# Performance work log

Measured on AMD Instinct MI355X. Metric: run time of the kernel, lower is better.

Reference implementation:

```python
import jax, jax.numpy as jnp
import numpy as np

B, T, C, K, V = 4, 4096, 128, 64, 64
EPS = 1e-5


def layer_norm(x, g, b):
    mu = jnp.mean(x, axis=-1, keepdims=True)
    var = jnp.var(x, axis=-1, keepdims=True)
    return (x - mu) * jax.lax.rsqrt(var + EPS) * g + b


def setup_inputs() -> dict:
    key = jax.random.key(0)
    ks = jax.random.split(key, 8)
    s = 1.0 / np.sqrt(C)
    return {
        "x": jax.random.normal(ks[0], (B, T, C), dtype=jnp.float32),
        "Wq": jax.random.uniform(ks[1], (C, K), jnp.float32, -s, s),
        "bq": jnp.zeros((K,), jnp.float32),
        "Wk": jax.random.uniform(ks[2], (C, K), jnp.float32, -s, s),
        "bk": jnp.zeros((K,), jnp.float32),
        "Wv": jax.random.uniform(ks[3], (C, V), jnp.float32, -s, s),
        "bv": jnp.zeros((V,), jnp.float32),
        "gq": jnp.ones((K,), jnp.float32), "bgq": jnp.zeros((K,), jnp.float32),
        "gk": jnp.ones((K,), jnp.float32), "bgk": jnp.zeros((K,), jnp.float32),
        "gv": jnp.ones((V,), jnp.float32), "bgv": jnp.zeros((V,), jnp.float32),
        "go": jnp.ones((V,), jnp.float32), "bgo": jnp.zeros((V,), jnp.float32),
    }


def reference(x, Wq, bq, Wk, bk, Wv, bv, gq, bgq, gk, bgk, gv, bgv, go, bgo):
    # projections: B x T x {K,K,V}
    q = layer_norm(x @ Wq + bq, gq, bgq)
    k = layer_norm(x @ Wk + bk, gk, bgk)
    v = layer_norm(x @ Wv + bv, gv, bgv)
    sqrt_k = jnp.asarray(np.sqrt(K), x.dtype)
    # full B x T x T causal score matrix (faithful to the original bmm+mask)
    logits = jnp.einsum("btk,bsk->bts", q, k) / sqrt_k
    t = jnp.arange(T)
    causal = t[:, None] >= t[None, :]  # lower-triangular incl. diagonal
    logits = jnp.where(causal[None], logits, -jnp.inf)
    probs = jax.nn.softmax(logits, axis=-1)
    read = jnp.einsum("bts,bsv->btv", probs, v)
    read = layer_norm(read, go, bgo)
    return jnp.concatenate([x, read], axis=2)  # B x T x (C+V)
```

## Files before the change

kernel.cpp:

```cpp
#include <hip/hip_runtime.h>

#define TT 4096

typedef unsigned short u16;
typedef unsigned int u32;

typedef short bf16x8 __attribute__((ext_vector_type(8)));
typedef float f32x4 __attribute__((ext_vector_type(4)));

union U8 {
  uint2 q[2];
  uint4 u4;
  bf16x8 v;
  short s[8];
  u32 w[4];
};

static __device__ __forceinline__ u16 f2bf(float f) {
  union { float f; u32 u; } cv;
  cv.f = f;
  u32 r = cv.u + 0x7FFFu + ((cv.u >> 16) & 1u);
  return (u16)(r >> 16);
}
static __device__ __forceinline__ u32 pk2(float a, float b) {
  return (u32)f2bf(a) | ((u32)f2bf(b) << 16);
}
static __device__ __forceinline__ float bf2f(u16 h) {
  union { u32 u; float f; } cv;
  cv.u = ((u32)h) << 16;
  return cv.f;
}
static __device__ __forceinline__ float exp2a(float x) {
  float r; asm("v_exp_f32 %0, %1" : "=v"(r) : "v"(x)); return r;
}
static __device__ __forceinline__ u32 cvtpk(float lo, float hi) {
  u32 r; asm("v_cvt_pk_bf16_f32 %0, %1, %2" : "=v"(r) : "v"(lo), "v"(hi)); return r;
}

__global__ __launch_bounds__(64)
void wpack(const float* __restrict__ Wq, const float* __restrict__ Wk,
           const float* __restrict__ Wv, u16* __restrict__ wf)
{
  const int g = blockIdx.x;
  const int p = g >> 4, s = (g >> 2) & 3, nt = g & 3;
  const int l = threadIdx.x, lg = l >> 4, l15 = l & 15;
  const float* W = (p == 0) ? Wq : (p == 1) ? Wk : Wv;
  const int n = l15 + 16 * nt;
  U8 o;
#pragma unroll
  for (int j = 0; j < 8; ++j) {
    int k = 32 * s + ((j < 4) ? (4 * lg + j) : (16 + 4 * lg + (j - 4)));
    o.s[j] = (short)f2bf(W[k * 64 + n]);
  }
  *(uint4*)(wf + (size_t)(g * 64 + l) * 8) = o.u4;
}

__global__ __launch_bounds__(256)
void proj_mfma(const float* __restrict__ x, const u16* __restrict__ wf,
               const float* __restrict__ bq, const float* __restrict__ bk,
               const float* __restrict__ bv,
               const float* __restrict__ gq, const float* __restrict__ bgq,
               const float* __restrict__ gk, const float* __restrict__ bgk,
               const float* __restrict__ gv, const float* __restrict__ bgv,
               u16* __restrict__ qo, u16* __restrict__ ko, u16* __restrict__ vto,
               float* __restrict__ out)
{
  __shared__ u16 xs[64 * 130];
  const int bx = blockIdx.x;
  const int xcd = bx & 7, i = bx >> 3;
  const int tile = xcd * 32 + (i & 31);
  const int p = i >> 5;
  const int rowbase = tile * 64;
  const int t = threadIdx.x;

  {
    const int row = t >> 2, seg = t & 3;
    const float4* src = (const float4*)(x + (size_t)(rowbase + row) * 128 + seg * 32);
    float4 f[8];
#pragma unroll
    for (int q = 0; q < 8; ++q) f[q] = src[q];
    if ((p == 0 && seg < 2) || (p == 1 && seg >= 2)) {
      float4* dst = (float4*)(out + (size_t)(rowbase + row) * 192 + seg * 32);
#pragma unroll
      for (int q = 0; q < 8; ++q) dst[q] = f[q];
    }
    const int base = row * 256 + seg * 64;
    const int swz = (row & 7) << 4;
    char* xb = (char*)xs;
#pragma unroll
    for (int q = 0; q < 4; ++q) {
      uint4 u;
      u.x = pk2(f[2 * q].x, f[2 * q].y);
      u.y = pk2(f[2 * q].z, f[2 * q].w);
      u.z = pk2(f[2 * q + 1].x, f[2 * q + 1].y);
      u.w = pk2(f[2 * q + 1].z, f[2 * q + 1].w);
      *(uint4*)(xb + ((base + 16 * q) ^ swz)) = u;
    }
  }

  const int w = t >> 6, l = t & 63, lg = l >> 4, l15 = l & 15;
  U8 bfr[4][4];
  const u16* wp = wf + (size_t)p * (16 * 64 * 8);
#pragma unroll
  for (int s = 0; s < 4; ++s)
#pragma unroll
    for (int nt = 0; nt < 4; ++nt)
      bfr[s][nt].u4 = *(const uint4*)(wp + ((s * 4 + nt) * 64 + l) * 8);

  __syncthreads();

  f32x4 acc[4];
#pragma unroll
  for (int nt = 0; nt < 4; ++nt) acc[nt] = (f32x4){0.f, 0.f, 0.f, 0.f};
  const int abase = (16 * w + l15) * 256;
  const int aswz = (l15 & 7) << 4;
  const char* xb = (const char*)xs;
#pragma unroll
  for (int s = 0; s < 4; ++s) {
    U8 af;
    af.q[0] = *(const uint2*)(xb + ((abase + s * 64 + 8 * lg) ^ aswz));
    af.q[1] = *(const uint2*)(xb + ((abase + s * 64 + 8 * lg + 32) ^ aswz));
#pragma unroll
    for (int nt = 0; nt < 4; ++nt)
      acc[nt] = __builtin_amdgcn_mfma_f32_16x16x32_bf16(af.v, bfr[s][nt].v, acc[nt], 0, 0, 0);
  }

  const float* bb = (p == 0) ? bq : (p == 1) ? bk : bv;
  const float* gg = (p == 0) ? gq : (p == 1) ? gk : gv;
  const float* hh = (p == 0) ? bgq : (p == 1) ? bgk : bgv;
  float bcol[4], gcol[4], hcol[4];
#pragma unroll
  for (int nt = 0; nt < 4; ++nt) {
    int col = l15 + 16 * nt;
    bcol[nt] = bb[col]; gcol[nt] = gg[col]; hcol[nt] = hh[col];
  }
  float vals[4][4];
#pragma unroll
  for (int nt = 0; nt < 4; ++nt)
#pragma unroll
    for (int r = 0; r < 4; ++r) vals[nt][r] = acc[nt][r] + bcol[nt];

  float s1[4], s2[4];
#pragma unroll
  for (int r = 0; r < 4; ++r) {
    s1[r] = vals[0][r] + vals[1][r] + vals[2][r] + vals[3][r];
    s2[r] = vals[0][r] * vals[0][r] + vals[1][r] * vals[1][r]
          + vals[2][r] * vals[2][r] + vals[3][r] * vals[3][r];
#pragma unroll
    for (int d = 1; d < 16; d <<= 1) {
      s1[r] += __shfl_xor(s1[r], d);
      s2[r] += __shfl_xor(s2[r], d);
    }
  }

  if (p < 2) {
    u16* dst = (p == 0) ? qo : ko;
#pragma unroll
    for (int r = 0; r < 4; ++r) {
      float mu = s1[r] * (1.f / 64.f);
      float var = s2[r] * (1.f / 64.f) - mu * mu;
      float rs = rsqrtf(var + 1e-5f);
      int grow = rowbase + 16 * w + 4 * lg + r;
#pragma unroll
      for (int nt = 0; nt < 4; ++nt)
        dst[(size_t)grow * 64 + l15 + 16 * nt] =
            f2bf((vals[nt][r] - mu) * rs * gcol[nt] + hcol[nt]);
    }
  } else {
    u16* vls = xs;
    __syncthreads();
#pragma unroll
    for (int r = 0; r < 4; ++r) {
      float mu = s1[r] * (1.f / 64.f);
      float var = s2[r] * (1.f / 64.f) - mu * mu;
      float rs = rsqrtf(var + 1e-5f);
      int row = 16 * w + 4 * lg + r;
#pragma unroll
      for (int nt = 0; nt < 4; ++nt)
        vls[row * 65 + l15 + 16 * nt] =
            f2bf((vals[nt][r] - mu) * rs * gcol[nt] + hcol[nt]);
    }
    __syncthreads();
    const int b = rowbase >> 12;
    const int tl = rowbase & 4095;
    const int col = t >> 2;
    const int tq = (t & 3) * 16;
    U8 o0, o1;
#pragma unroll
    for (int i = 0; i < 8; ++i) o0.s[i] = (short)vls[(tq + i) * 65 + col];
#pragma unroll
    for (int i = 0; i < 8; ++i) o1.s[i] = (short)vls[(tq + 8 + i) * 65 + col];
    u16* dst = vto + (size_t)(b * 64 + col) * TT + tl + tq;
    *(uint4*)(dst + 0) = o0.u4;
    *(uint4*)(dst + 8) = o1.u4;
  }
}

__global__ __launch_bounds__(256)
void attn_seg4p(const u16* __restrict__ qg, const u16* __restrict__ kg,
                const u16* __restrict__ vtg,
                float* __restrict__ lP, u16* __restrict__ aP)
{
  __shared__ u16 kl4[4 * 64 * 64];
  __shared__ u16 vl4[4 * 64 * 64];
  const int bx = blockIdx.x;
  const int xcd = bx & 7, b = xcd >> 1, e2 = xcd & 1;
  const int j = e2 * 272 + (bx >> 3);
  int Q = 0;
  while (2 * (Q + 1) * (Q + 2) <= j) ++Q;
  const int ip = j - 2 * Q * (Q + 1);
  const int dv = ip / (Q + 1);
  const int q = 4 * Q + dv;
  const int s = ip - dv * (Q + 1);
  const int q0 = q * 64;
  const int it0 = s * 4;
  const int it1 = min(it0 + 4, q + 1);

  const int t = threadIdx.x;
  const int w = t >> 6, l = t & 63;
  const int l15 = l & 15, lg = l >> 4;
  const int swzl = (l15 & 7) << 4;

  const int wbase = q0 + 16 * w;
  const int qrow = wbase + l15;
  const u16* qrp = qg + (size_t)(b * TT + qrow) * 64;
  U8 qf[2];
#pragma unroll
  for (int hh = 0; hh < 2; ++hh) {
    qf[hh].q[0] = *(const uint2*)(qrp + 32 * hh + 4 * lg);
    qf[hh].q[1] = *(const uint2*)(qrp + 32 * hh + 4 * lg + 16);
  }

  {
    const int key = t >> 2, part = t & 3;
    const int sbase = key * 128 + part * 32;
    const int ssw = (key & 7) << 4;
    uint4 kr[4][2], vr[4][2];
#pragma unroll
    for (int tt = 0; tt < 4; ++tt) {
      int tile = it0 + tt; if (tile >= it1) tile = it1 - 1;
      const u16* ks = kg + (size_t)(b * TT + tile * 64 + key) * 64 + part * 16;
      kr[tt][0] = ((const uint4*)ks)[0];
      kr[tt][1] = ((const uint4*)ks)[1];
      const u16* vs = vtg + (size_t)(b * 64 + key) * TT + tile * 64 + part * 16;
      vr[tt][0] = ((const uint4*)vs)[0];
      vr[tt][1] = ((const uint4*)vs)[1];
    }
#pragma unroll
    for (int tt = 0; tt < 4; ++tt) {
      char* kd = (char*)kl4 + tt * 8192;
      char* vd = (char*)vl4 + tt * 8192;
      *(uint4*)(kd + ((sbase + 0) ^ ssw)) = kr[tt][0];
      *(uint4*)(kd + ((sbase + 16) ^ ssw)) = kr[tt][1];
      *(uint4*)(vd + ((sbase + 0) ^ ssw)) = vr[tt][0];
      *(uint4*)(vd + ((sbase + 16) ^ ssw)) = vr[tt][1];
    }
  }
  __syncthreads();

  const float C = 0.18033688011112042f;
  float l_run = 0.f;
  f32x4 acc[4];
#pragma unroll
  for (int ct = 0; ct < 4; ++ct) acc[ct] = (f32x4){0.f, 0.f, 0.f, 0.f};

#define QK_TILE(ST, TOF)                                                      \
  {                                                                           \
    const char* kp_ = (const char*)kl4 + (TOF);                               \
    _Pragma("unroll")                                                         \
    for (int t4 = 0; t4 < 4; ++t4) {                                          \
      const int rbase = (16 * t4 + l15) * 128 + 8 * lg;                       \
      U8 kf0, kf1;                                                            \
      kf0.q[0] = *(const uint2*)(kp_ + ((rbase + 0) ^ swzl));                 \
      kf0.q[1] = *(const uint2*)(kp_ + ((rbase + 32) ^ swzl));                \
      kf1.q[0] = *(const uint2*)(kp_ + ((rbase + 64) ^ swzl));                \
      kf1.q[1] = *(const uint2*)(kp_ + ((rbase + 96) ^ swzl));                \
      f32x4 d_ = {0.f, 0.f, 0.f, 0.f};                                       \
      d_ = __builtin_amdgcn_mfma_f32_16x16x32_bf16(kf0.v, qf[0].v, d_, 0, 0, 0); \
      d_ = __builtin_amdgcn_mfma_f32_16x16x32_bf16(kf1.v, qf[1].v, d_, 0, 0, 0); \
      ST[t4] = d_;                                                            \
    }                                                                         \
  }

  f32x4 stC[4];
  QK_TILE(stC, 0);

  int toff = 0;
  for (int it = it0; it < it1; ++it, toff += 8192) {
    const int kb = it * 64;
    const bool have_next = (it + 1 < it1);

    f32x4 stN[4];
    if (have_next) QK_TILE(stN, toff + 8192);

    const char* vp = (const char*)vl4 + toff;
    U8 vf[4][2];
#pragma unroll
    for (int ct = 0; ct < 4; ++ct) {
      const int vb = (16 * ct + l15) * 128 + 8 * lg;
#pragma unroll
      for (int u = 0; u < 2; ++u) {
        vf[ct][u].q[0] = *(const uint2*)(vp + ((vb + 64 * u + 0) ^ swzl));
        vf[ct][u].q[1] = *(const uint2*)(vp + ((vb + 64 * u + 32) ^ swzl));
      }
    }

    float p[16];
    const bool needmask = (kb + 63 > wbase);
    if (needmask) {
#pragma unroll
      for (int t4 = 0; t4 < 4; ++t4) {
#pragma unroll
        for (int r = 0; r < 4; ++r) {
          int keyidx = kb + 16 * t4 + 4 * lg + r;
          float e = exp2a(stC[t4][r] * C);
          p[t4 * 4 + r] = (keyidx > qrow) ? 0.f : e;
        }
      }
    } else {
#pragma unroll
      for (int t4 = 0; t4 < 4; ++t4) {
#pragma unroll
        for (int r = 0; r < 4; ++r) p[t4 * 4 + r] = exp2a(stC[t4][r] * C);
      }
    }
    float sm[8];
#pragma unroll
    for (int i = 0; i < 8; ++i) sm[i] = p[2 * i] + p[2 * i + 1];
#pragma unroll
    for (int i = 0; i < 4; ++i) sm[i] = sm[2 * i] + sm[2 * i + 1];
    float rsum = (sm[0] + sm[1]) + (sm[2] + sm[3]);
    rsum += __shfl_xor(rsum, 16);
    rsum += __shfl_xor(rsum, 32);
    l_run += rsum;

    U8 pa[2];
#pragma unroll
    for (int u = 0; u < 2; ++u) {
#pragma unroll
      for (int k2 = 0; k2 < 4; ++k2)
        pa[u].w[k2] = cvtpk(p[8 * u + 2 * k2], p[8 * u + 2 * k2 + 1]);
    }

    __builtin_amdgcn_s_setprio(1);
#pragma unroll
    for (int ct = 0; ct < 4; ++ct) {
#pragma unroll
      for (int u = 0; u < 2; ++u)
        acc[ct] = __builtin_amdgcn_mfma_f32_16x16x32_bf16(pa[u].v, vf[ct][u].v, acc[ct], 0, 0, 0);
    }
    __builtin_amdgcn_s_setprio(0);

    if (have_next) {
#pragma unroll
      for (int t4 = 0; t4 < 4; ++t4) stC[t4] = stN[t4];
    }
  }
#undef QK_TILE

  const size_t pbase = (size_t)(b * 544 + j) * 64;
  if (lg == 0) lP[pbase + 16 * w + l15] = l_run;
#pragma unroll
  for (int ct = 0; ct < 4; ++ct) {
#pragma unroll
    for (int r = 0; r < 4; ++r) {
      int rin = 16 * w + 4 * lg + r;
      aP[(pbase + rin) * 64 + l15 + 16 * ct] = f2bf(acc[ct][r]);
    }
  }
}

__global__ __launch_bounds__(256)
void attn_merge4n(const float* __restrict__ lP, const u16* __restrict__ aP,
                  const float* __restrict__ go, const float* __restrict__ bgo,
                  float* __restrict__ out)
{
  const int t = threadIdx.x;
  const int w = t >> 6, c = t & 63;
  const int row = blockIdx.x * 4 + w;
  const int tid2 = row >> 6, rin = row & 63;
  const int b = tid2 >> 6, q = tid2 & 63;
  const int Q = q >> 2;
  const int base_q = b * 544 + 2 * Q * (Q + 1) + (q & 3) * (Q + 1);
  const int ns = Q + 1;

  float L = 0.f, o = 0.f;
  for (int s = 0; s < ns; ++s) {
    const size_t pb = (size_t)(base_q + s) * 64;
    L += lP[pb + rin];
    o += bf2f(aP[(pb + rin) * 64 + c]);
  }
  o /= L;

  float s1 = o, s2 = o * o;
#pragma unroll
  for (int d = 1; d < 64; d <<= 1) {
    s1 += __shfl_xor(s1, d);
    s2 += __shfl_xor(s2, d);
  }
  float mu = s1 * (1.f / 64.f);
  float var = s2 * (1.f / 64.f) - mu * mu;
  float rs = rsqrtf(var + 1e-5f);
  out[(size_t)row * 192 + 128 + c] = (o - mu) * rs * go[c] + bgo[c];
}

__global__ __launch_bounds__(128)
void attn1(const u16* __restrict__ qg, const u16* __restrict__ kg,
           const u16* __restrict__ vtg,
           const float* __restrict__ go, const float* __restrict__ bgo,
           float* __restrict__ out)
{
  __shared__ u16 kl[64 * 64];
  __shared__ u16 vl[64 * 64];
  const int bx = blockIdx.x;
  const int tt = (bx < 256) ? bx : (767 - bx);
  const int b = tt >> 7;
  const int q0 = (tt & 127) * 32;
  const int tid = threadIdx.x;
  const int w = tid >> 6;
  const int l = tid & 63;
  const int l15 = l & 15;
  const int lg = l >> 4;
  const int swzl = (l15 & 7) << 4;

  const int qrow = q0 + 16 * w + l15;
  const u16* qrp = qg + (size_t)(b * TT + qrow) * 64;
  U8 qf[2];
#pragma unroll
  for (int h = 0; h < 2; ++h) {
    qf[h].q[0] = *(const uint2*)(qrp + 32 * h + 4 * lg);
    qf[h].q[1] = *(const uint2*)(qrp + 32 * h + 4 * lg + 16);
  }

  float m_run = -1e30f, l_run = 0.f;
  f32x4 acc[4];
#pragma unroll
  for (int ct = 0; ct < 4; ++ct) acc[ct] = (f32x4){0.f, 0.f, 0.f, 0.f};

  const int nkv = (q0 >> 6) + 1;
  for (int it = 0; it < nkv; ++it) {
    const int kb = it * 64;
    {
      const int key = tid >> 1;
      const int dh = (tid & 1) * 32;
      const u16* ks = kg + (size_t)(b * TT + kb + key) * 64 + dh;
      uint4 d0 = *(const uint4*)(ks + 0);
      uint4 d1 = *(const uint4*)(ks + 8);
      uint4 d2 = *(const uint4*)(ks + 16);
      uint4 d3 = *(const uint4*)(ks + 24);
      const int base = key * 128 + dh * 2;
      const int sw = (key & 7) << 4;
      char* kd = (char*)kl;
      *(uint4*)(kd + ((base + 0) ^ sw)) = d0;
      *(uint4*)(kd + ((base + 16) ^ sw)) = d1;
      *(uint4*)(kd + ((base + 32) ^ sw)) = d2;
      *(uint4*)(kd + ((base + 48) ^ sw)) = d3;
      const u16* vs = vtg + (size_t)(b * 64 + key) * TT + kb + dh;
      uint4 e0 = *(const uint4*)(vs + 0);
      uint4 e1 = *(const uint4*)(vs + 8);
      uint4 e2 = *(const uint4*)(vs + 16);
      uint4 e3 = *(const uint4*)(vs + 24);
      char* vd = (char*)vl;
      *(uint4*)(vd + ((base + 0) ^ sw)) = e0;
      *(uint4*)(vd + ((base + 16) ^ sw)) = e1;
      *(uint4*)(vd + ((base + 32) ^ sw)) = e2;
      *(uint4*)(vd + ((base + 48) ^ sw)) = e3;
    }
    __syncthreads();

    f32x4 st[4];
#pragma unroll
    for (int t4 = 0; t4 < 4; ++t4) {
      const int rbase = (16 * t4 + l15) * 128 + 8 * lg;
      const char* kp = (const char*)kl;
      U8 kf0, kf1;
      kf0.q[0] = *(const uint2*)(kp + ((rbase + 0) ^ swzl));
      kf0.q[1] = *(const uint2*)(kp + ((rbase + 32) ^ swzl));
      kf1.q[0] = *(const uint2*)(kp + ((rbase + 64) ^ swzl));
      kf1.q[1] = *(const uint2*)(kp + ((rbase + 96) ^ swzl));
      f32x4 d = {0.f, 0.f, 0.f, 0.f};
      d = __builtin_amdgcn_mfma_f32_16x16x32_bf16(kf0.v, qf[0].v, d, 0, 0, 0);
      d = __builtin_amdgcn_mfma_f32_16x16x32_bf16(kf1.v, qf[1].v, d, 0, 0, 0);
      st[t4] = d;
    }

    float sv[16];
    const bool needmask = (kb + 63 > q0 + 16 * w);
#pragma unroll
    for (int t4 = 0; t4 < 4; ++t4) {
#pragma unroll
      for (int r = 0; r < 4; ++r) {
        float sc = st[t4][r] * 0.125f;
        if (needmask) {
          int keyidx = kb + 16 * t4 + 4 * lg + r;
          if (keyidx > qrow) sc = -1e30f;
        }
        sv[t4 * 4 + r] = sc;
      }
    }
    float mt = sv[0];
#pragma unroll
    for (int i = 1; i < 16; ++i) mt = fmaxf(mt, sv[i]);
    mt = fmaxf(mt, __shfl_xor(mt, 16));
    mt = fmaxf(mt, __shfl_xor(mt, 32));
    const float mnew = fmaxf(m_run, mt);
    const float al = __expf(m_run - mnew);
    float p[16];
    float rsum = 0.f;
#pragma unroll
    for (int i = 0; i < 16; ++i) { p[i] = __expf(sv[i] - mnew); rsum += p[i]; }
    rsum += __shfl_xor(rsum, 16);
    rsum += __shfl_xor(rsum, 32);
    l_run = l_run * al + rsum;
    m_run = mnew;
    float ar[4];
#pragma unroll
    for (int r = 0; r < 4; ++r) ar[r] = __shfl(al, 4 * lg + r);
#pragma unroll
    for (int ct = 0; ct < 4; ++ct) {
#pragma unroll
      for (int r = 0; r < 4; ++r) acc[ct][r] *= ar[r];
    }
    U8 pa[2];
#pragma unroll
    for (int u = 0; u < 2; ++u) {
#pragma unroll
      for (int i = 0; i < 8; ++i) pa[u].s[i] = (short)f2bf(p[8 * u + i]);
    }

#pragma unroll
    for (int ct = 0; ct < 4; ++ct) {
      const int vb = (16 * ct + l15) * 128 + 8 * lg;
      const char* vp = (const char*)vl;
#pragma unroll
      for (int u = 0; u < 2; ++u) {
        U8 vf;
        vf.q[0] = *(const uint2*)(vp + ((vb + 64 * u + 0) ^ swzl));
        vf.q[1] = *(const uint2*)(vp + ((vb + 64 * u + 32) ^ swzl));
        acc[ct] = __builtin_amdgcn_mfma_f32_16x16x32_bf16(pa[u].v, vf.v, acc[ct], 0, 0, 0);
      }
    }
    __syncthreads();
  }

  float linv[4];
#pragma unroll
  for (int r = 0; r < 4; ++r) linv[r] = 1.f / __shfl(l_run, 4 * lg + r);
  float o[4][4];
#pragma unroll
  for (int ct = 0; ct < 4; ++ct) {
#pragma unroll
    for (int r = 0; r < 4; ++r) o[ct][r] = acc[ct][r] * linv[r];
  }
  float s1[4], s2[4];
#pragma unroll
  for (int r = 0; r < 4; ++r) {
    s1[r] = o[0][r] + o[1][r] + o[2][r] + o[3][r];
    s2[r] = o[0][r] * o[0][r] + o[1][r] * o[1][r] + o[2][r] * o[2][r] + o[3][r] * o[3][r];
#pragma unroll
    for (int d = 1; d < 16; d <<= 1) {
      s1[r] += __shfl_xor(s1[r], d);
      s2[r] += __shfl_xor(s2[r], d);
    }
  }
  float gov[4], bgv2[4];
#pragma unroll
  for (int ct = 0; ct < 4; ++ct) {
    gov[ct] = go[16 * ct + l15];
    bgv2[ct] = bgo[16 * ct + l15];
  }
#pragma unroll
  for (int r = 0; r < 4; ++r) {
    float mu = s1[r] * (1.f / 64.f);
    float var = s2[r] * (1.f / 64.f) - mu * mu;
    float rs = rsqrtf(var + 1e-5f);
    int row = q0 + 16 * w + 4 * lg + r;
    float* op = out + (size_t)(b * TT + row) * 192 + 128;
#pragma unroll
    for (int ct = 0; ct < 4; ++ct)
      op[16 * ct + l15] = (o[ct][r] - mu) * rs * gov[ct] + bgv2[ct];
  }
}

extern "C" void kernel_launch(void* const* d_in, const int* in_sizes, int n_in,
                              void* d_out, int out_size, void* d_ws, size_t ws_size,
                              hipStream_t stream) {
  (void)in_sizes; (void)n_in; (void)out_size;
  const float* x   = (const float*)d_in[0];
  const float* Wq  = (const float*)d_in[1];
  const float* bq  = (const float*)d_in[2];
  const float* Wk  = (const float*)d_in[3];
  const float* bk  = (const float*)d_in[4];
  const float* Wv  = (const float*)d_in[5];
  const float* bv  = (const float*)d_in[6];
  const float* gq  = (const float*)d_in[7];
  const float* bgq = (const float*)d_in[8];
  const float* gk  = (const float*)d_in[9];
  const float* bgk = (const float*)d_in[10];
  const float* gv  = (const float*)d_in[11];
  const float* bgv = (const float*)d_in[12];
  const float* go  = (const float*)d_in[13];
  const float* bgo = (const float*)d_in[14];
  float* out = (float*)d_out;

  char* wsb = (char*)d_ws;
  u16* qws  = (u16*)wsb;
  u16* kws  = (u16*)(wsb + (2u << 20));
  u16* vtws = (u16*)(wsb + (4u << 20));
  u16* wfr  = (u16*)(wsb + (6u << 20));
  const size_t OFF_LP = (6u << 20) + 65536;

  wpack<<<48, 64, 0, stream>>>(Wq, Wk, Wv, wfr);
  proj_mfma<<<768, 256, 0, stream>>>(x, wfr, bq, bk, bv,
                                     gq, bgq, gk, bgk, gv, bgv,
                                     qws, kws, vtws, out);

  {
    const size_t SEG4 = 4u * 544;
    const size_t LPS = SEG4 * 64 * 4;
    const size_t APS = SEG4 * 64 * 64 * 2;
    const size_t OFF_AP = OFF_LP + LPS;
    const size_t NEED = OFF_AP + APS;

    if (ws_size >= NEED) {
      float* lP = (float*)(wsb + OFF_LP);
      u16*   aP = (u16*)(wsb + OFF_AP);
      attn_seg4p<<<2176, 256, 0, stream>>>(qws, kws, vtws, lP, aP);
      attn_merge4n<<<4096, 256, 0, stream>>>(lP, aP, go, bgo, out);
    } else {
      attn1<<<512, 128, 0, stream>>>(qws, kws, vtws, go, bgo, out);
    }
  }
}
```

Baseline: 63.27 us.

## Process two query tiles per block to reuse staged K/V tiles

Each attention block now handles a pair of adjacent 64-row query tiles that share the same 4-tile key segment, so K/V staged into LDS and the K/V fragment reads feed twice as many MFMAs. The grid halves and the segment indexing is remapped so partial results still land in the same slots the merge kernel expects. The software-pipelined prefetch of the next QK tile is dropped in favour of independent A/B MFMA streams for latency hiding. The trade-off is doubled accumulator and register pressure, fewer blocks for occupancy and load balance, and some masked work in the lower tile of each pair.

```diff
diff --git a/kernel.cpp b/kernel.cpp
--- a/kernel.cpp
+++ b/kernel.cpp
@@ -197,38 +197,41 @@
 }
 
 __global__ __launch_bounds__(256)
-void attn_seg4p(const u16* __restrict__ qg, const u16* __restrict__ kg,
-                const u16* __restrict__ vtg,
-                float* __restrict__ lP, u16* __restrict__ aP)
+void attn_pair4n(const u16* __restrict__ qg, const u16* __restrict__ kg,
+                 const u16* __restrict__ vtg,
+                 float* __restrict__ lP, u16* __restrict__ aP)
 {
   __shared__ u16 kl4[4 * 64 * 64];
   __shared__ u16 vl4[4 * 64 * 64];
   const int bx = blockIdx.x;
   const int xcd = bx & 7, b = xcd >> 1, e2 = xcd & 1;
-  const int j = e2 * 272 + (bx >> 3);
-  int Q = 0;
-  while (2 * (Q + 1) * (Q + 2) <= j) ++Q;
-  const int ip = j - 2 * Q * (Q + 1);
-  const int dv = ip / (Q + 1);
-  const int q = 4 * Q + dv;
-  const int s = ip - dv * (Q + 1);
-  const int q0 = q * 64;
-  const int it0 = s * 4;
-  const int it1 = min(it0 + 4, q + 1);
+  const int j = e2 * 136 + (bx >> 3);
+  int M = 0;
+  while ((M + 1) * (M + 2) <= j) ++M;
+  const int ip = j - M * (M + 1);
+  const int e = (ip >= M + 1) ? 1 : 0;
+  const int s = ip - e * (M + 1);
+  const int pr = 2 * M + e;
+  const int qa = 2 * pr, qb = 2 * pr + 1;
+  const int it0 = 4 * s;
+  const int it1 = min(it0 + 4, qb + 1);
 
   const int t = threadIdx.x;
   const int w = t >> 6, l = t & 63;
   const int l15 = l & 15, lg = l >> 4;
   const int swzl = (l15 & 7) << 4;
 
-  const int wbase = q0 + 16 * w;
-  const int qrow = wbase + l15;
-  const u16* qrp = qg + (size_t)(b * TT + qrow) * 64;
-  U8 qf[2];
+  const int wbaseA = qa * 64 + 16 * w, wbaseB = qb * 64 + 16 * w;
+  const int qrowA = wbaseA + l15, qrowB = wbaseB + l15;
+  const u16* qrpA = qg + (size_t)(b * TT + qrowA) * 64;
+  const u16* qrpB = qg + (size_t)(b * TT + qrowB) * 64;
+  U8 qfA[2], qfB[2];
 #pragma unroll
   for (int hh = 0; hh < 2; ++hh) {
-    qf[hh].q[0] = *(const uint2*)(qrp + 32 * hh + 4 * lg);
-    qf[hh].q[1] = *(const uint2*)(qrp + 32 * hh + 4 * lg + 16);
+    qfA[hh].q[0] = *(const uint2*)(qrpA + 32 * hh + 4 * lg);
+    qfA[hh].q[1] = *(const uint2*)(qrpA + 32 * hh + 4 * lg + 16);
+    qfB[hh].q[0] = *(const uint2*)(qrpB + 32 * hh + 4 * lg);
+    qfB[hh].q[1] = *(const uint2*)(qrpB + 32 * hh + 4 * lg + 16);
   }
 
   {
@@ -259,113 +262,139 @@
   __syncthreads();
 
   const float C = 0.18033688011112042f;
-  float l_run = 0.f;
-  f32x4 acc[4];
-#pragma unroll
-  for (int ct = 0; ct < 4; ++ct) acc[ct] = (f32x4){0.f, 0.f, 0.f, 0.f};
-
-#define QK_TILE(ST, TOF)                                                      \
-  {                                                                           \
-    const char* kp_ = (const char*)kl4 + (TOF);                               \
-    _Pragma("unroll")                                                         \
-    for (int t4 = 0; t4 < 4; ++t4) {                                          \
-      const int rbase = (16 * t4 + l15) * 128 + 8 * lg;                       \
-      U8 kf0, kf1;                                                            \
-      kf0.q[0] = *(const uint2*)(kp_ + ((rbase + 0) ^ swzl));                 \
-      kf0.q[1] = *(const uint2*)(kp_ + ((rbase + 32) ^ swzl));                \
-      kf1.q[0] = *(const uint2*)(kp_ + ((rbase + 64) ^ swzl));                \
-      kf1.q[1] = *(const uint2*)(kp_ + ((rbase + 96) ^ swzl));                \
-      f32x4 d_ = {0.f, 0.f, 0.f, 0.f};                                       \
-      d_ = __builtin_amdgcn_mfma_f32_16x16x32_bf16(kf0.v, qf[0].v, d_, 0, 0, 0); \
-      d_ = __builtin_amdgcn_mfma_f32_16x16x32_bf16(kf1.v, qf[1].v, d_, 0, 0, 0); \
-      ST[t4] = d_;                                                            \
-    }                                                                         \
-  }
-
-  f32x4 stC[4];
-  QK_TILE(stC, 0);
+  float lA = 0.f, lB = 0.f;
+  f32x4 accA[4], accB[4];
+#pragma unroll
+  for (int ct = 0; ct < 4; ++ct) {
+    accA[ct] = (f32x4){0.f, 0.f, 0.f, 0.f};
+    accB[ct] = (f32x4){0.f, 0.f, 0.f, 0.f};
+  }
 
   int toff = 0;
   for (int it = it0; it < it1; ++it, toff += 8192) {
     const int kb = it * 64;
-    const bool have_next = (it + 1 < it1);
-
-    f32x4 stN[4];
-    if (have_next) QK_TILE(stN, toff + 8192);
-
+    const char* kp = (const char*)kl4 + toff;
     const char* vp = (const char*)vl4 + toff;
-    U8 vf[4][2];
+
+    f32x4 stA[4], stB[4];
+    __builtin_amdgcn_s_setprio(1);
+#pragma unroll
+    for (int t4 = 0; t4 < 4; ++t4) {
+      const int rbase = (16 * t4 + l15) * 128 + 8 * lg;
+      U8 kf0, kf1;
+      kf0.q[0] = *(const uint2*)(kp + ((rbase + 0) ^ swzl));
+      kf0.q[1] = *(const uint2*)(kp + ((rbase + 32) ^ swzl));
+      kf1.q[0] = *(const uint2*)(kp + ((rbase + 64) ^ swzl));
+      kf1.q[1] = *(const uint2*)(kp + ((rbase + 96) ^ swzl));
+      f32x4 dA = {0.f, 0.f, 0.f, 0.f};
+      dA = __builtin_amdgcn_mfma_f32_16x16x32_bf16(kf0.v, qfA[0].v, dA, 0, 0, 0);
+      dA = __builtin_amdgcn_mfma_f32_16x16x32_bf16(kf1.v, qfA[1].v, dA, 0, 0, 0);
+      stA[t4] = dA;
+      f32x4 dB = {0.f, 0.f, 0.f, 0.f};
+      dB = __builtin_amdgcn_mfma_f32_16x16x32_bf16(kf0.v, qfB[0].v, dB, 0, 0, 0);
+      dB = __builtin_amdgcn_mfma_f32_16x16x32_bf16(kf1.v, qfB[1].v, dB, 0, 0, 0);
+      stB[t4] = dB;
+    }
+    __builtin_amdgcn_s_setprio(0);
+
+    float pA[16], pB[16];
+    const bool maskA = (kb + 63 > wbaseA);
+    if (maskA) {
+#pragma unroll
+      for (int t4 = 0; t4 < 4; ++t4) {
+#pragma unroll
+        for (int r = 0; r < 4; ++r) {
+          int keyidx = kb + 16 * t4 + 4 * lg + r;
+          float e = exp2a(stA[t4][r] * C);
+          pA[t4 * 4 + r] = (keyidx > qrowA) ? 0.f : e;
+        }
+      }
+    } else {
+#pragma unroll
+      for (int t4 = 0; t4 < 4; ++t4) {
+#pragma unroll
+        for (int r = 0; r < 4; ++r) pA[t4 * 4 + r] = exp2a(stA[t4][r] * C);
+      }
+    }
+    const bool maskB = (kb + 63 > wbaseB);
+    if (maskB) {
+#pragma unroll
+      for (int t4 = 0; t4 < 4; ++t4) {
+#pragma unroll
+        for (int r = 0; r < 4; ++r) {
+          int keyidx = kb + 16 * t4 + 4 * lg + r;
+          float e = exp2a(stB[t4][r] * C);
+          pB[t4 * 4 + r] = (keyidx > qrowB) ? 0.f : e;
+        }
+      }
+    } else {
+#pragma unroll
+      for (int t4 = 0; t4 < 4; ++t4) {
+#pragma unroll
+        for (int r = 0; r < 4; ++r) pB[t4 * 4 + r] = exp2a(stB[t4][r] * C);
+      }
+    }
+    float smA[8], smB[8];
+#pragma unroll
+    for (int i = 0; i < 8; ++i) {
+      smA[i] = pA[2 * i] + pA[2 * i + 1];
+      smB[i] = pB[2 * i] + pB[2 * i + 1];
+    }
+#pragma unroll
+    for (int i = 0; i < 4; ++i) {
+      smA[i] = smA[2 * i] + smA[2 * i + 1];
+      smB[i] = smB[2 * i] + smB[2 * i + 1];
+    }
+    float rsA = (smA[0] + smA[1]) + (smA[2] + smA[3]);
+    float rsB = (smB[0] + smB[1]) + (smB[2] + smB[3]);
+    rsA += __shfl_xor(rsA, 16);
+    rsB += __shfl_xor(rsB, 16);
+    rsA += __shfl_xor(rsA, 32);
+    rsB += __shfl_xor(rsB, 32);
+    lA += rsA;
+    lB += rsB;
+
+    U8 paA[2], paB[2];
+#pragma unroll
+    for (int u = 0; u < 2; ++u) {
+#pragma unroll
+      for (int k2 = 0; k2 < 4; ++k2) {
+        paA[u].w[k2] = cvtpk(pA[8 * u + 2 * k2], pA[8 * u + 2 * k2 + 1]);
+        paB[u].w[k2] = cvtpk(pB[8 * u + 2 * k2], pB[8 * u + 2 * k2 + 1]);
+      }
+    }
+
+    __builtin_amdgcn_s_setprio(1);
 #pragma unroll
     for (int ct = 0; ct < 4; ++ct) {
       const int vb = (16 * ct + l15) * 128 + 8 * lg;
 #pragma unroll
       for (int u = 0; u < 2; ++u) {
-        vf[ct][u].q[0] = *(const uint2*)(vp + ((vb + 64 * u + 0) ^ swzl));
-        vf[ct][u].q[1] = *(const uint2*)(vp + ((vb + 64 * u + 32) ^ swzl));
-      }
-    }
-
-    float p[16];
-    const bool needmask = (kb + 63 > wbase);
-    if (needmask) {
-#pragma unroll
-      for (int t4 = 0; t4 < 4; ++t4) {
-#pragma unroll
-        for (int r = 0; r < 4; ++r) {
-          int keyidx = kb + 16 * t4 + 4 * lg + r;
-          float e = exp2a(stC[t4][r] * C);
-          p[t4 * 4 + r] = (keyidx > qrow) ? 0.f : e;
-        }
-      }
-    } else {
-#pragma unroll
-      for (int t4 = 0; t4 < 4; ++t4) {
-#pragma unroll
-        for (int r = 0; r < 4; ++r) p[t4 * 4 + r] = exp2a(stC[t4][r] * C);
-      }
-    }
-    float sm[8];
-#pragma unroll
-    for (int i = 0; i < 8; ++i) sm[i] = p[2 * i] + p[2 * i + 1];
-#pragma unroll
-    for (int i = 0; i < 4; ++i) sm[i] = sm[2 * i] + sm[2 * i + 1];
-    float rsum = (sm[0] + sm[1]) + (sm[2] + sm[3]);
-    rsum += __shfl_xor(rsum, 16);
-    rsum += __shfl_xor(rsum, 32);
-    l_run += rsum;
-
-    U8 pa[2];
-#pragma unroll
-    for (int u = 0; u < 2; ++u) {
-#pragma unroll
-      for (int k2 = 0; k2 < 4; ++k2)
-        pa[u].w[k2] = cvtpk(p[8 * u + 2 * k2], p[8 * u + 2 * k2 + 1]);
-    }
-
-    __builtin_amdgcn_s_setprio(1);
-#pragma unroll
-    for (int ct = 0; ct < 4; ++ct) {
-#pragma unroll
-      for (int u = 0; u < 2; ++u)
-        acc[ct] = __builtin_amdgcn_mfma_f32_16x16x32_bf16(pa[u].v, vf[ct][u].v, acc[ct], 0, 0, 0);
+        U8 vf;
+        vf.q[0] = *(const uint2*)(vp + ((vb + 64 * u + 0) ^ swzl));
+        vf.q[1] = *(const uint2*)(vp + ((vb + 64 * u + 32) ^ swzl));
+        accA[ct] = __builtin_amdgcn_mfma_f32_16x16x32_bf16(paA[u].v, vf.v, accA[ct], 0, 0, 0);
+        accB[ct] = __builtin_amdgcn_mfma_f32_16x16x32_bf16(paB[u].v, vf.v, accB[ct], 0, 0, 0);
+      }
     }
     __builtin_amdgcn_s_setprio(0);
-
-    if (have_next) {
-#pragma unroll
-      for (int t4 = 0; t4 < 4; ++t4) stC[t4] = stN[t4];
-    }
-  }
-#undef QK_TILE
-
-  const size_t pbase = (size_t)(b * 544 + j) * 64;
-  if (lg == 0) lP[pbase + 16 * w + l15] = l_run;
+  }
+
+  const int jqA = 2 * M * (M + 1) + (2 * e) * (M + 1) + s;
+  const int jqB = 2 * M * (M + 1) + (2 * e + 1) * (M + 1) + s;
+  const size_t pbA = (size_t)(b * 544 + jqA) * 64;
+  const size_t pbB = (size_t)(b * 544 + jqB) * 64;
+  if (lg == 0) {
+    lP[pbA + 16 * w + l15] = lA;
+    lP[pbB + 16 * w + l15] = lB;
+  }
 #pragma unroll
   for (int ct = 0; ct < 4; ++ct) {
 #pragma unroll
     for (int r = 0; r < 4; ++r) {
       int rin = 16 * w + 4 * lg + r;
-      aP[(pbase + rin) * 64 + l15 + 16 * ct] = f2bf(acc[ct][r]);
+      aP[(pbA + rin) * 64 + l15 + 16 * ct] = f2bf(accA[ct][r]);
+      aP[(pbB + rin) * 64 + l15 + 16 * ct] = f2bf(accB[ct][r]);
     }
   }
 }
@@ -625,7 +654,7 @@
     if (ws_size >= NEED) {
       float* lP = (float*)(wsb + OFF_LP);
       u16*   aP = (u16*)(wsb + OFF_AP);
-      attn_seg4p<<<2176, 256, 0, stream>>>(qws, kws, vtws, lP, aP);
+      attn_pair4n<<<1088, 256, 0, stream>>>(qws, kws, vtws, lP, aP);
       attn_merge4n<<<4096, 256, 0, stream>>>(lP, aP, go, bgo, out);
     } else {
       attn1<<<512, 128, 0, stream>>>(qws, kws, vtws, go, bgo, out);
```

Result: faster. 59.02 us, median of 2 (-6.7%).
